# Optimization experiments

Hardware: AMD Instinct MI355X
Metric: run time of the kernel (lower is better)

The kernel has to match this reference:

```python
import jax, jax.numpy as jnp
import numpy as np

B, T, D = 8, 2048, 256  # batch, time segments, feature dim (a_dim=v_dim=hidden=out=256)
EPS = 1e-8


def _layer_norm(x, g, b, eps=1e-6):
    m = jnp.mean(x, axis=-1, keepdims=True)
    v = jnp.var(x, axis=-1, keepdims=True)
    return (x - m) * jax.lax.rsqrt(v + eps) * g + b


def setup_inputs() -> dict:
    key = jax.random.key(0)
    ks = jax.random.split(key, 9)
    xav = lambda k: jax.random.uniform(k, (D, D), jnp.float32, -1.0, 1.0) * np.sqrt(6.0 / (D + D))
    return {
        "a_fea": jax.random.normal(ks[0], (B, T, D), jnp.float32),
        "v_fea": jax.random.normal(ks[1], (B, T, D), jnp.float32),
        "thr_val": jnp.float32(0.099),
        "Wv1": xav(ks[2]), "Wv2": xav(ks[3]), "Wvfc": xav(ks[4]),
        "Wa1": xav(ks[5]), "Wa2": xav(ks[6]), "Wafc": xav(ks[7]),
        "ln_g": jnp.ones((D,), jnp.float32),
        "ln_b": jnp.zeros((D,), jnp.float32),
    }


def reference(a_fea, v_fea, thr_val, Wv1, Wv2, Wvfc, Wa1, Wa2, Wafc, ln_g, ln_b):
    relu = jax.nn.relu
    # branch projections (dropout is identity at eval); torch Linear: x @ W.T
    v1 = relu(jnp.einsum('btd,hd->bth', v_fea, Wv1))
    v2 = relu(jnp.einsum('btd,hd->bth', v_fea, Wv2))
    a1 = relu(jnp.einsum('btd,hd->bth', a_fea, Wa1))
    a2 = relu(jnp.einsum('btd,hd->bth', a_fea, Wa2))

    d = v2.shape[-1]
    # scaled cross-modal scores, ReLU'd  [B, Tv, Ta]
    beta_va = relu(jnp.einsum('btd,bsd->bts', v2, a1) / jnp.sqrt(jnp.float32(d)))
    # a->v scores taken BEFORE row-normalization of beta_va (as in torch code)
    beta_av = jnp.transpose(beta_va, (0, 2, 1))

    time = beta_va.shape[-1]
    thr = thr_val * 10.0 / time

    # normalize -> threshold sparsify -> renormalize (v attends to a)
    bn_va = beta_va / (jnp.sum(beta_va, axis=-1, keepdims=True) + EPS)
    g_va = jnp.where(bn_va > thr, bn_va, 0.0)
    g_va = g_va / (jnp.sum(g_va, axis=-1, keepdims=True) + EPS)

    # same for a attends to v
    bn_av = beta_av / (jnp.sum(beta_av, axis=-1, keepdims=True) + EPS)
    g_av = jnp.where(bn_av > thr, bn_av, 0.0)
    g_av = g_av / (jnp.sum(g_av, axis=-1, keepdims=True) + EPS)

    # vectorized form of the diagonal selection double-loop (batch element 0)
    pred = (jnp.diagonal(g_av[0]) > 0).astype(jnp.float32)  # [T]

    a_pos = jnp.einsum('bts,bsd->btd', g_va, a2)
    v_psp = v_fea + a_pos
    v_pos = jnp.einsum('bts,bsd->btd', g_av, v1)
    a_psp = a_fea + v_pos

    v_psp = _layer_norm(relu(jnp.einsum('btd,od->bto', v_psp, Wvfc)), ln_g, ln_b)
    a_psp = _layer_norm(relu(jnp.einsum('btd,od->bto', a_psp, Wafc)), ln_g, ln_b)
    a_v_fuse = 0.5 * (v_psp + a_psp)
    return a_v_fuse, v_psp, a_psp, pred
```

## Files before the change

### kernel.cpp

```cpp
#include <hip/hip_runtime.h>
#include <math.h>

#define TT 2048
#define DD 256
#define NBATCH 8
#define EPSF 1e-8f

typedef unsigned short u16;
typedef __attribute__((ext_vector_type(8))) short short8;
typedef __attribute__((ext_vector_type(4))) float f32x4;

__device__ __forceinline__ u16 f2bf(float x) {
    unsigned int u = __builtin_bit_cast(unsigned int, x);
    u += 0x7fffu + ((u >> 16) & 1u);
    return (u16)(u >> 16);
}
__device__ __forceinline__ float bf2f(u16 h) {
    return __builtin_bit_cast(float, (unsigned int)h << 16);
}

__device__ __forceinline__ int frag_dst(int row, int k) {
    return (((row >> 4) * 4 + (k >> 3)) * 16 + (row & 15)) * 8 + (k & 7);
}

template<int BR>
__device__ __forceinline__ void stage_tile(const u16* __restrict__ g, u16* s,
                                           int row0, int k0, int ldk, int tid)
{
    #pragma unroll
    for (int i = 0; i < BR / 64; ++i) {
        const int c = tid + 256 * i;
        const int row = c >> 2, q = c & 3;
        *(int4*)(s + frag_dst(row, q * 8)) =
            *(const int4*)(g + (long)(row0 + row) * ldk + k0 + q * 8);
    }
}

__global__ __launch_bounds__(256)
void proj_kernel(const u16* __restrict__ vfh, const u16* __restrict__ vfl,
                 const u16* __restrict__ afh, const u16* __restrict__ afl,
                 const u16* __restrict__ Wsp,
                 u16* __restrict__ v2h, u16* __restrict__ v2l,
                 u16* __restrict__ a1h, u16* __restrict__ a1l,
                 u16* __restrict__ v1T, u16* __restrict__ a2T)
{
    const int zz = blockIdx.z;
    const u16* Ah = (zz == 1 || zz == 3) ? afh : vfh;
    const u16* Al = (zz == 1 || zz == 3) ? afl : vfl;
    const int widx = (zz == 0) ? 2 : (zz == 1) ? 4 : (zz == 2) ? 0 : 6;
    const u16* Bh = Wsp + widx * DD * DD;
    const u16* Bl = Bh + DD * DD;
    const bool split = zz < 2;
    u16* Oh = (zz == 0) ? v2h : a1h;
    u16* Ol = (zz == 0) ? v2l : a1l;
    u16* OT = (zz == 2) ? v1T : a2T;

    __shared__ __align__(16) u16 Ah_s[64 * 32], Al_s[64 * 32];
    __shared__ __align__(16) u16 Bh_s[64 * 32], Bl_s[64 * 32];
    const int m0 = blockIdx.y * 64, n0 = blockIdx.x * 64;
    const int tid = threadIdx.x, lane = tid & 63, w = tid >> 6;
    const int wy = w >> 1, wx = w & 1;
    f32x4 acc[2][2] = {};

    for (int k0 = 0; k0 < DD; k0 += 32) {
        stage_tile<64>(Ah, Ah_s, m0, k0, DD, tid);
        stage_tile<64>(Al, Al_s, m0, k0, DD, tid);
        stage_tile<64>(Bh, Bh_s, n0, k0, DD, tid);
        stage_tile<64>(Bl, Bl_s, n0, k0, DD, tid);
        __syncthreads();
        short8 ah[2], al[2], bh[2], bl[2];
        #pragma unroll
        for (int i = 0; i < 2; ++i) {
            ah[i] = *(const short8*)(Ah_s + ((wy * 2 + i) * 64 + lane) * 8);
            al[i] = *(const short8*)(Al_s + ((wy * 2 + i) * 64 + lane) * 8);
        }
        #pragma unroll
        for (int j = 0; j < 2; ++j) {
            bh[j] = *(const short8*)(Bh_s + ((wx * 2 + j) * 64 + lane) * 8);
            bl[j] = *(const short8*)(Bl_s + ((wx * 2 + j) * 64 + lane) * 8);
        }
        #pragma unroll
        for (int i = 0; i < 2; ++i)
            #pragma unroll
            for (int j = 0; j < 2; ++j) {
                acc[i][j] = __builtin_amdgcn_mfma_f32_16x16x32_bf16(ah[i], bl[j], acc[i][j], 0, 0, 0);
                acc[i][j] = __builtin_amdgcn_mfma_f32_16x16x32_bf16(al[i], bh[j], acc[i][j], 0, 0, 0);
                acc[i][j] = __builtin_amdgcn_mfma_f32_16x16x32_bf16(ah[i], bh[j], acc[i][j], 0, 0, 0);
            }
        __syncthreads();
    }
    const int quad = lane >> 4, col = lane & 15;
    #pragma unroll
    for (int i = 0; i < 2; ++i)
        #pragma unroll
        for (int j = 0; j < 2; ++j) {
            const int c = n0 + (wx * 2 + j) * 16 + col;
            const int rbase = m0 + (wy * 2 + i) * 16 + quad * 4;
            if (split) {
                #pragma unroll
                for (int r = 0; r < 4; ++r) {
                    const float v = fmaxf(acc[i][j][r], 0.f);
                    const u16 h = f2bf(v);
                    Oh[(long)(rbase + r) * DD + c] = h;
                    Ol[(long)(rbase + r) * DD + c] = f2bf(v - bf2f(h));
                }
            } else {
                short4 pk;
                pk.x = (short)f2bf(fmaxf(acc[i][j][0], 0.f));
                pk.y = (short)f2bf(fmaxf(acc[i][j][1], 0.f));
                pk.z = (short)f2bf(fmaxf(acc[i][j][2], 0.f));
                pk.w = (short)f2bf(fmaxf(acc[i][j][3], 0.f));
                const int b = rbase >> 11, t = rbase & (TT - 1);
                *(short4*)(OT + ((long)b * DD + c) * TT + t) = pk;
            }
        }
}

__global__ __launch_bounds__(256)
void score_kernel(const u16* __restrict__ v2h, const u16* __restrict__ v2l,
                  const u16* __restrict__ a1h, const u16* __restrict__ a1l,
                  u16* __restrict__ beta, u16* __restrict__ betaT,
                  float* __restrict__ rs, float* __restrict__ cs)
{
    __shared__ __align__(16) u16 S[128 * 136];
    u16* Ah_s = S;
    u16* Al_s = S + 4096;
    u16* Bh_s = S + 8192;
    u16* Bl_s = S + 12288;
    const int z = blockIdx.z;
    const int m0 = blockIdx.y * 128, n0 = blockIdx.x * 128;
    const int tid = threadIdx.x, lane = tid & 63, w = tid >> 6;
    const int wy = w >> 1, wx = w & 1;
    const long zoff = (long)z * TT * DD;
    f32x4 acc[4][4] = {};

    for (int k0 = 0; k0 < DD; k0 += 32) {
        stage_tile<128>(v2h + zoff, Ah_s, m0, k0, DD, tid);
        stage_tile<128>(v2l + zoff, Al_s, m0, k0, DD, tid);
        stage_tile<128>(a1h + zoff, Bh_s, n0, k0, DD, tid);
        stage_tile<128>(a1l + zoff, Bl_s, n0, k0, DD, tid);
        __syncthreads();
        short8 ah[4], al[4], bh[4], bl[4];
        #pragma unroll
        for (int i = 0; i < 4; ++i) {
            ah[i] = *(const short8*)(Ah_s + ((wy * 4 + i) * 64 + lane) * 8);
            al[i] = *(const short8*)(Al_s + ((wy * 4 + i) * 64 + lane) * 8);
        }
        #pragma unroll
        for (int j = 0; j < 4; ++j) {
            bh[j] = *(const short8*)(Bh_s + ((wx * 4 + j) * 64 + lane) * 8);
            bl[j] = *(const short8*)(Bl_s + ((wx * 4 + j) * 64 + lane) * 8);
        }
        #pragma unroll
        for (int i = 0; i < 4; ++i)
            #pragma unroll
            for (int j = 0; j < 4; ++j) {
                acc[i][j] = __builtin_amdgcn_mfma_f32_16x16x32_bf16(ah[i], bl[j], acc[i][j], 0, 0, 0);
                acc[i][j] = __builtin_amdgcn_mfma_f32_16x16x32_bf16(al[i], bh[j], acc[i][j], 0, 0, 0);
                acc[i][j] = __builtin_amdgcn_mfma_f32_16x16x32_bf16(ah[i], bh[j], acc[i][j], 0, 0, 0);
            }
        __syncthreads();
    }

    const int quad = lane >> 4, col = lane & 15;
    const float scale = 1.f / 16.f;
    #pragma unroll
    for (int i = 0; i < 4; ++i)
        #pragma unroll
        for (int j = 0; j < 4; ++j) {
            const int c = n0 + (wx * 4 + j) * 16 + col;
            const int rbase = m0 + (wy * 4 + i) * 16 + quad * 4;
            #pragma unroll
            for (int r = 0; r < 4; ++r) {
                float v = fmaxf(acc[i][j][r] * scale, 0.f);
                acc[i][j][r] = v;
                beta[((long)z * TT + rbase + r) * TT + c] = f2bf(v);
            }
        }
    #pragma unroll
    for (int i = 0; i < 4; ++i)
        #pragma unroll
        for (int r = 0; r < 4; ++r) {
            float rp = 0.f;
            #pragma unroll
            for (int j = 0; j < 4; ++j) rp += acc[i][j][r];
            rp += __shfl_xor(rp, 1); rp += __shfl_xor(rp, 2);
            rp += __shfl_xor(rp, 4); rp += __shfl_xor(rp, 8);
            if (col == 0) {
                const int row = m0 + (wy * 4 + i) * 16 + quad * 4 + r;
                atomicAdd(&rs[(long)z * TT + row], rp);
            }
        }
    #pragma unroll
    for (int j = 0; j < 4; ++j) {
        float cp = 0.f;
        #pragma unroll
        for (int i = 0; i < 4; ++i)
            #pragma unroll
            for (int r = 0; r < 4; ++r) cp += acc[i][j][r];
        cp += __shfl_xor(cp, 16); cp += __shfl_xor(cp, 32);
        if (lane < 16) {
            const int c = n0 + (wx * 4 + j) * 16 + col;
            atomicAdd(&cs[(long)z * TT + c], cp);
        }
    }
    __syncthreads();
    #pragma unroll
    for (int i = 0; i < 4; ++i)
        #pragma unroll
        for (int j = 0; j < 4; ++j) {
            const int cl = (wx * 4 + j) * 16 + col;
            const int rl = (wy * 4 + i) * 16 + quad * 4;
            short4 pk;
            pk.x = (short)f2bf(acc[i][j][0]);
            pk.y = (short)f2bf(acc[i][j][1]);
            pk.z = (short)f2bf(acc[i][j][2]);
            pk.w = (short)f2bf(acc[i][j][3]);
            *(short4*)(S + cl * 136 + rl) = pk;
        }
    __syncthreads();
    #pragma unroll
    for (int it = 0; it < 8; ++it) {
        const int idx = tid + 256 * it;
        const int cl = idx >> 4, tq = idx & 15;
        const int4 v = *(const int4*)(S + cl * 136 + tq * 8);
        *(int4*)(betaT + ((long)z * TT + n0 + cl) * TT + m0 + tq * 8) = v;
    }
}

__global__ __launch_bounds__(512)
void pv_kernel(const u16* __restrict__ beta, const u16* __restrict__ betaT,
               const u16* __restrict__ a2T, const u16* __restrict__ v1T,
               const float* __restrict__ rs, const float* __restrict__ cs,
               const float* __restrict__ thrp,
               const float* __restrict__ v_fea, const float* __restrict__ a_fea,
               u16* __restrict__ yvin, u16* __restrict__ yain)
{
    __shared__ __align__(16) u16 A_s[128 * 32], B_s[256 * 32];
    __shared__ float sthr[128], sA[128], ssum[128];
    const int zz = blockIdx.x;
    const int m0 = blockIdx.y * 128;
    const int z = zz & 7;
    const bool av = zz >= 8;
    const u16* P      = av ? betaT : beta;
    const u16* VT     = av ? v1T : a2T;
    const float* sums = av ? cs : rs;
    const float* resid = av ? a_fea : v_fea;
    u16* outb         = av ? yain : yvin;

    const int tid = threadIdx.x, lane = tid & 63, w = tid >> 6;
    const int wy = w >> 2, wx = w & 3;
    const float thr = thrp[0] * 10.0f / (float)TT;
    if (tid < 128) {
        const float s = sums[(long)z * TT + m0 + tid];
        sA[tid] = s; sthr[tid] = thr * (s + EPSF); ssum[tid] = 0.f;
    }
    __syncthreads();
    f32x4 acc[4][4] = {};
    float rpart = 0.f;
    const int arow = tid >> 2, aq = tid & 3;
    const u16* Pp = P + ((long)z * TT + m0 + arow) * TT + aq * 8;
    const u16* V0 = VT + (long)z * DD * TT + (long)arow * TT + aq * 8;
    const u16* V1 = V0 + (long)128 * TT;

    int4 Ar  = *(const int4*)(Pp);
    int4 Br0 = *(const int4*)(V0);
    int4 Br1 = *(const int4*)(V1);

    for (int k0 = 0; k0 < TT; k0 += 32) {
        union { int4 v; u16 us[8]; } U;
        U.v = Ar;
        const float ct = sthr[arow];
        float ss = 0.f;
        #pragma unroll
        for (int t = 0; t < 8; ++t) {
            const float v = bf2f(U.us[t]);
            if (v > ct) ss += v; else U.us[t] = 0;
        }
        rpart += ss;
        *(int4*)(A_s + frag_dst(arow, aq * 8)) = U.v;
        *(int4*)(B_s + frag_dst(arow, aq * 8)) = Br0;
        *(int4*)(B_s + frag_dst(arow + 128, aq * 8)) = Br1;
        __syncthreads();
        const int kn = (k0 + 32 < TT) ? (k0 + 32) : k0;
        Ar  = *(const int4*)(Pp + kn);
        Br0 = *(const int4*)(V0 + kn);
        Br1 = *(const int4*)(V1 + kn);
        short8 a[4], b[4];
        #pragma unroll
        for (int i = 0; i < 4; ++i)
            a[i] = *(const short8*)(A_s + ((wy * 4 + i) * 64 + lane) * 8);
        #pragma unroll
        for (int j = 0; j < 4; ++j)
            b[j] = *(const short8*)(B_s + ((wx * 4 + j) * 64 + lane) * 8);
        #pragma unroll
        for (int i = 0; i < 4; ++i)
            #pragma unroll
            for (int j = 0; j < 4; ++j)
                acc[i][j] = __builtin_amdgcn_mfma_f32_16x16x32_bf16(a[i], b[j], acc[i][j], 0, 0, 0);
        __syncthreads();
    }
    atomicAdd(&ssum[arow], rpart);
    __syncthreads();

    const int quad = lane >> 4, col = lane & 15;
    #pragma unroll
    for (int i = 0; i < 4; ++i)
        #pragma unroll
        for (int j = 0; j < 4; ++j) {
            const int c = (wx * 4 + j) * 16 + col;
            #pragma unroll
            for (int r = 0; r < 4; ++r) {
                const int lrow = (wy * 4 + i) * 16 + quad * 4 + r;
                const int row = m0 + lrow;
                const float inv = 1.0f / (ssum[lrow] + EPSF * (sA[lrow] + EPSF));
                const float v = acc[i][j][r] * inv + resid[((long)z * TT + row) * DD + c];
                outb[((long)z * TT + row) * DD + c] = f2bf(v);
            }
        }
}

__global__ __launch_bounds__(256)
void fc_kernel(const u16* __restrict__ Ain, const u16* __restrict__ Wb,
               float* __restrict__ Cf)
{
    const int z = blockIdx.z;
    const u16* A = Ain + (size_t)z * (size_t)NBATCH * TT * DD;
    const u16* B = Wb + (size_t)z * DD * DD;
    float* C = Cf + (size_t)z * (size_t)NBATCH * TT * DD;
    __shared__ __align__(16) u16 A_s[128 * 32], B_s[64 * 32];
    const int m0 = blockIdx.y * 128, n0 = blockIdx.x * 64;
    const int tid = threadIdx.x, lane = tid & 63, w = tid >> 6;
    const int wy = w >> 1, wx = w & 1;
    f32x4 acc[4][2] = {};
    for (int k0 = 0; k0 < DD; k0 += 32) {
        stage_tile<128>(A, A_s, m0, k0, DD, tid);
        stage_tile<64>(B, B_s, n0, k0, DD, tid);
        __syncthreads();
        short8 a[4], b[2];
        #pragma unroll
        for (int i = 0; i < 4; ++i)
            a[i] = *(const short8*)(A_s + ((wy * 4 + i) * 64 + lane) * 8);
        #pragma unroll
        for (int j = 0; j < 2; ++j)
            b[j] = *(const short8*)(B_s + ((wx * 2 + j) * 64 + lane) * 8);
        #pragma unroll
        for (int i = 0; i < 4; ++i)
            #pragma unroll
            for (int j = 0; j < 2; ++j)
                acc[i][j] = __builtin_amdgcn_mfma_f32_16x16x32_bf16(a[i], b[j], acc[i][j], 0, 0, 0);
        __syncthreads();
    }
    const int quad = lane >> 4, col = lane & 15;
    #pragma unroll
    for (int i = 0; i < 4; ++i)
        #pragma unroll
        for (int j = 0; j < 2; ++j) {
            const int c = n0 + (wx * 2 + j) * 16 + col;
            #pragma unroll
            for (int r = 0; r < 4; ++r) {
                const int row = m0 + (wy * 4 + i) * 16 + quad * 4 + r;
                C[(long)row * DD + c] = fmaxf(acc[i][j][r], 0.f);
            }
        }
}

__global__ __launch_bounds__(256)
void pred_exact(const float* __restrict__ vf, const float* __restrict__ af,
                const float* __restrict__ Wv2, const float* __restrict__ Wa1,
                const float* __restrict__ cs, const float* __restrict__ thrp,
                float* __restrict__ pred)
{
    __shared__ float vs[8][260];
    __shared__ float as_[8][260];
    __shared__ float red[4][8];
    const int t0 = blockIdx.x * 8;
    const int tid = threadIdx.x;
    {
        const int i = tid >> 5, c = (tid & 31) * 8;
        *(float4*)&vs[i][c] = *(const float4*)(vf + (long)(t0 + i) * DD + c);
        *(float4*)&vs[i][c + 4] = *(const float4*)(vf + (long)(t0 + i) * DD + c + 4);
        *(float4*)&as_[i][c] = *(const float4*)(af + (long)(t0 + i) * DD + c);
        *(float4*)&as_[i][c + 4] = *(const float4*)(af + (long)(t0 + i) * DD + c + 4);
    }
    __syncthreads();
    const int j = tid;
    float av[8] = {0.f}, aa[8] = {0.f};
    for (int k = 0; k < DD; k += 4) {
        const float4 wv = *(const float4*)(Wv2 + (long)j * DD + k);
        const float4 wa = *(const float4*)(Wa1 + (long)j * DD + k);
        #pragma unroll
        for (int i = 0; i < 8; ++i) {
            const float4 x = *(const float4*)&vs[i][k];
            av[i] += wv.x * x.x + wv.y * x.y + wv.z * x.z + wv.w * x.w;
            const float4 y = *(const float4*)&as_[i][k];
            aa[i] += wa.x * y.x + wa.y * y.y + wa.z * y.z + wa.w * y.w;
        }
    }
    float p[8];
    #pragma unroll
    for (int i = 0; i < 8; ++i)
        p[i] = fmaxf(av[i], 0.f) * fmaxf(aa[i], 0.f);
    #pragma unroll
    for (int off = 32; off > 0; off >>= 1)
        #pragma unroll
        for (int i = 0; i < 8; ++i) p[i] += __shfl_xor(p[i], off);
    const int lane = tid & 63, wv_ = tid >> 6;
    if (lane == 0)
        #pragma unroll
        for (int i = 0; i < 8; ++i) red[wv_][i] = p[i];
    __syncthreads();
    if (tid < 8) {
        float d = red[0][tid] + red[1][tid] + red[2][tid] + red[3][tid];
        d = fmaxf(d * (1.f / 16.f), 0.f);
        const float thr = thrp[0] * 10.0f / (float)TT;
        pred[t0 + tid] = (d > thr * (cs[t0 + tid] + EPSF)) ? 1.0f : 0.0f;
    }
}

__global__ __launch_bounds__(256)
void split_feat(const float* __restrict__ vf, const float* __restrict__ af,
                u16* __restrict__ vfh, u16* __restrict__ vfl,
                u16* __restrict__ afh, u16* __restrict__ afl)
{
    const long i4 = ((long)blockIdx.x * 256 + threadIdx.x) * 4;
    const float* src = blockIdx.y ? af : vf;
    u16* dh = blockIdx.y ? afh : vfh;
    u16* dl = blockIdx.y ? afl : vfl;
    float4 a = *(const float4*)(src + i4);
    ushort4 h4, l4; u16 h;
    h = f2bf(a.x); h4.x = h; l4.x = f2bf(a.x - bf2f(h));
    h = f2bf(a.y); h4.y = h; l4.y = f2bf(a.y - bf2f(h));
    h = f2bf(a.z); h4.z = h; l4.z = f2bf(a.z - bf2f(h));
    h = f2bf(a.w); h4.w = h; l4.w = f2bf(a.w - bf2f(h));
    *(ushort4*)(dh + i4) = h4;
    *(ushort4*)(dl + i4) = l4;
}

__global__ __launch_bounds__(256)
void split_w(const float* __restrict__ w0, const float* __restrict__ w1,
             const float* __restrict__ w2, const float* __restrict__ w3,
             const float* __restrict__ w4, const float* __restrict__ w5,
             u16* __restrict__ out)
{
    const int t = blockIdx.y;
    const float* w = (t == 0) ? w0 : (t == 1) ? w1 : (t == 2) ? w2
                   : (t == 3) ? w3 : (t == 4) ? w4 : w5;
    const int i4 = (blockIdx.x * 256 + threadIdx.x) * 4;
    float4 a = *(const float4*)(w + i4);
    if (t < 4) {
        u16* oh = out + (size_t)t * 2 * DD * DD;
        u16* ol = oh + DD * DD;
        ushort4 h4, l4; u16 h;
        h = f2bf(a.x); h4.x = h; l4.x = f2bf(a.x - bf2f(h));
        h = f2bf(a.y); h4.y = h; l4.y = f2bf(a.y - bf2f(h));
        h = f2bf(a.z); h4.z = h; l4.z = f2bf(a.z - bf2f(h));
        h = f2bf(a.w); h4.w = h; l4.w = f2bf(a.w - bf2f(h));
        *(ushort4*)(oh + i4) = h4;
        *(ushort4*)(ol + i4) = l4;
    } else {
        u16* ob = out + (size_t)8 * DD * DD + (size_t)(t - 4) * DD * DD;
        ushort4 o;
        o.x = f2bf(a.x); o.y = f2bf(a.y); o.z = f2bf(a.z); o.w = f2bf(a.w);
        *(ushort4*)(ob + i4) = o;
    }
}

__global__ __launch_bounds__(256)
void ln_fuse_kernel(const float* __restrict__ yv, const float* __restrict__ ya,
                    const float* __restrict__ g, const float* __restrict__ b,
                    float* __restrict__ fuse, float* __restrict__ vpsp,
                    float* __restrict__ apsp)
{
    const long row = (long)blockIdx.x * 4 + (threadIdx.x >> 6);
    const int lane = threadIdx.x & 63;
    const float4 xv = *(const float4*)(yv + row * DD + lane * 4);
    const float4 xa = *(const float4*)(ya + row * DD + lane * 4);
    float sv = xv.x + xv.y + xv.z + xv.w;
    float sa = xa.x + xa.y + xa.z + xa.w;
    #pragma unroll
    for (int off = 32; off > 0; off >>= 1) {
        sv += __shfl_xor(sv, off);
        sa += __shfl_xor(sa, off);
    }
    const float mv = sv * (1.f / 256.f);
    const float ma = sa * (1.f / 256.f);
    const float dv0 = xv.x - mv, dv1 = xv.y - mv, dv2 = xv.z - mv, dv3 = xv.w - mv;
    const float da0 = xa.x - ma, da1 = xa.y - ma, da2 = xa.z - ma, da3 = xa.w - ma;
    float qv = dv0 * dv0 + dv1 * dv1 + dv2 * dv2 + dv3 * dv3;
    float qa = da0 * da0 + da1 * da1 + da2 * da2 + da3 * da3;
    #pragma unroll
    for (int off = 32; off > 0; off >>= 1) {
        qv += __shfl_xor(qv, off);
        qa += __shfl_xor(qa, off);
    }
    const float rv = rsqrtf(qv * (1.f / 256.f) + 1e-6f);
    const float ra = rsqrtf(qa * (1.f / 256.f) + 1e-6f);
    const float4 gg = *(const float4*)(g + lane * 4);
    const float4 bb = *(const float4*)(b + lane * 4);
    float4 ov, oa, of;
    ov.x = dv0 * rv * gg.x + bb.x; ov.y = dv1 * rv * gg.y + bb.y;
    ov.z = dv2 * rv * gg.z + bb.z; ov.w = dv3 * rv * gg.w + bb.w;
    oa.x = da0 * ra * gg.x + bb.x; oa.y = da1 * ra * gg.y + bb.y;
    oa.z = da2 * ra * gg.z + bb.z; oa.w = da3 * ra * gg.w + bb.w;
    of.x = 0.5f * (ov.x + oa.x); of.y = 0.5f * (ov.y + oa.y);
    of.z = 0.5f * (ov.z + oa.z); of.w = 0.5f * (ov.w + oa.w);
    *(float4*)(vpsp + row * DD + lane * 4) = ov;
    *(float4*)(apsp + row * DD + lane * 4) = oa;
    *(float4*)(fuse + row * DD + lane * 4) = of;
}

extern "C" void kernel_launch(void* const* d_in, const int* in_sizes, int n_in,
                              void* d_out, int out_size, void* d_ws, size_t ws_size,
                              hipStream_t stream)
{
    const float* a_fea = (const float*)d_in[0];
    const float* v_fea = (const float*)d_in[1];
    const float* thrp  = (const float*)d_in[2];
    const float* Wv1   = (const float*)d_in[3];
    const float* Wv2   = (const float*)d_in[4];
    const float* Wvfc  = (const float*)d_in[5];
    const float* Wa1   = (const float*)d_in[6];
    const float* Wa2   = (const float*)d_in[7];
    const float* Wafc  = (const float*)d_in[8];
    const float* lng   = (const float*)d_in[9];
    const float* lnb   = (const float*)d_in[10];

    const long MT = (long)NBATCH * TT;
    float* out_fuse = (float*)d_out;
    float* out_vpsp = out_fuse + MT * DD;
    float* out_apsp = out_vpsp + MT * DD;
    float* out_pred = out_apsp + MT * DD;

    char* ws = (char*)d_ws;
    const size_t fb = (size_t)MT * DD * sizeof(u16);
    const size_t sumB = (size_t)MT * sizeof(float);
    u16* v2h  = (u16*)(ws + 0 * fb);
    u16* v2l  = (u16*)(ws + 1 * fb);
    u16* a1h  = (u16*)(ws + 2 * fb);
    u16* a1l  = (u16*)(ws + 3 * fb);
    u16* yvin = (u16*)(ws + 4 * fb);
    u16* yain = (u16*)(ws + 5 * fb);
    u16* v1T  = (u16*)(ws + 6 * fb);
    u16* a2T  = (u16*)(ws + 7 * fb);
    char* p = ws + 8 * fb;
    float* rs = (float*)(p + 0 * sumB);
    float* cs = (float*)(p + 1 * sumB);
    u16* Wsp  = (u16*)(p + 2 * sumB);
    char* q = p + 2 * sumB + 10 * DD * DD * sizeof(u16);
    const size_t betaB = (size_t)NBATCH * TT * TT * sizeof(u16);
    u16* beta  = (u16*)q;
    u16* betaT = (u16*)(q + betaB);
    u16* vfh = (u16*)q;
    u16* vfl = vfh + MT * DD;
    u16* afh = vfl + MT * DD;
    u16* afl = afh + MT * DD;
    float* yv = (float*)(ws + 0 * fb);
    float* ya = (float*)(ws + 2 * fb);

    hipMemsetAsync(rs, 0, 2 * sumB, stream);

    const dim3 blk(256, 1, 1);

    split_feat<<<dim3((unsigned)(MT * DD / 1024), 2, 1), blk, 0, stream>>>(
        v_fea, a_fea, vfh, vfl, afh, afl);
    split_w<<<dim3(DD * DD / 1024, 6, 1), blk, 0, stream>>>(
        Wv1, Wv2, Wa1, Wa2, Wvfc, Wafc, Wsp);

    proj_kernel<<<dim3(DD / 64, (unsigned)(MT / 64), 4), blk, 0, stream>>>(
        vfh, vfl, afh, afl, Wsp, v2h, v2l, a1h, a1l, v1T, a2T);

    score_kernel<<<dim3(TT / 128, TT / 128, NBATCH), blk, 0, stream>>>(
        v2h, v2l, a1h, a1l, beta, betaT, rs, cs);
    pred_exact<<<dim3(TT / 8, 1, 1), blk, 0, stream>>>(
        v_fea, a_fea, Wv2, Wa1, cs, thrp, out_pred);

    pv_kernel<<<dim3(2 * NBATCH, TT / 128, 1), dim3(512, 1, 1), 0, stream>>>(
        beta, betaT, a2T, v1T, rs, cs, thrp, v_fea, a_fea, yvin, yain);

    fc_kernel<<<dim3(DD / 64, (unsigned)(MT / 128), 2), blk, 0, stream>>>(
        yvin, Wsp + 8 * DD * DD, yv);
    ln_fuse_kernel<<<dim3((unsigned)(MT / 4), 1, 1), blk, 0, stream>>>(
        yv, ya, lng, lnb, out_fuse, out_vpsp, out_apsp);
}
```

Baseline: 443.4 us.

## Swizzle LDS fragment layout, prefetch score tiles in registers, stage beta stores

Adds an XOR swizzle to the LDS fragment layout, used consistently by every GEMM stage and read, to cut LDS bank conflicts on the int4 stores. The score kernel now preloads the next k-slice of its global tiles into registers while the MFMAs run on the current one, so loads overlap compute. It also writes the bf16 beta tile through LDS and then stores it with coalesced 16-byte rows, replacing scattered 2-byte stores. This costs more registers in the score kernel and one extra barrier.

```diff
diff --git a/kernel.cpp b/kernel.cpp
--- a/kernel.cpp
+++ b/kernel.cpp
@@ -23,6 +23,8 @@
     return (((row >> 4) * 4 + (k >> 3)) * 16 + (row & 15)) * 8 + (k & 7);
 }
 
+__device__ __forceinline__ int swz(int i) { return i ^ ((i >> 2) & 32); }
+
 template<int BR>
 __device__ __forceinline__ void stage_tile(const u16* __restrict__ g, u16* s,
                                            int row0, int k0, int ldk, int tid)
@@ -31,7 +33,7 @@
     for (int i = 0; i < BR / 64; ++i) {
         const int c = tid + 256 * i;
         const int row = c >> 2, q = c & 3;
-        *(int4*)(s + frag_dst(row, q * 8)) =
+        *(int4*)(s + swz(frag_dst(row, q * 8))) =
             *(const int4*)(g + (long)(row0 + row) * ldk + k0 + q * 8);
     }
 }
@@ -71,13 +73,13 @@
         short8 ah[2], al[2], bh[2], bl[2];
         #pragma unroll
         for (int i = 0; i < 2; ++i) {
-            ah[i] = *(const short8*)(Ah_s + ((wy * 2 + i) * 64 + lane) * 8);
-            al[i] = *(const short8*)(Al_s + ((wy * 2 + i) * 64 + lane) * 8);
+            ah[i] = *(const short8*)(Ah_s + swz(((wy * 2 + i) * 64 + lane) * 8));
+            al[i] = *(const short8*)(Al_s + swz(((wy * 2 + i) * 64 + lane) * 8));
         }
         #pragma unroll
         for (int j = 0; j < 2; ++j) {
-            bh[j] = *(const short8*)(Bh_s + ((wx * 2 + j) * 64 + lane) * 8);
-            bl[j] = *(const short8*)(Bl_s + ((wx * 2 + j) * 64 + lane) * 8);
+            bh[j] = *(const short8*)(Bh_s + swz(((wx * 2 + j) * 64 + lane) * 8));
+            bl[j] = *(const short8*)(Bl_s + swz(((wx * 2 + j) * 64 + lane) * 8));
         }
         #pragma unroll
         for (int i = 0; i < 2; ++i)
@@ -134,22 +136,41 @@
     const long zoff = (long)z * TT * DD;
     f32x4 acc[4][4] = {};
 
+    const int prow = tid >> 2, pq = tid & 3;
+    const int d0 = swz(frag_dst(prow, pq * 8));
+    const int d1 = swz(frag_dst(prow + 64, pq * 8));
+    const u16* gAh = v2h + zoff + (long)(m0 + prow) * DD + pq * 8;
+    const u16* gAl = v2l + zoff + (long)(m0 + prow) * DD + pq * 8;
+    const u16* gBh = a1h + zoff + (long)(n0 + prow) * DD + pq * 8;
+    const u16* gBl = a1l + zoff + (long)(n0 + prow) * DD + pq * 8;
+    const int rstep = 64 * DD;
+
+    int4 rAh0 = *(const int4*)(gAh), rAh1 = *(const int4*)(gAh + rstep);
+    int4 rAl0 = *(const int4*)(gAl), rAl1 = *(const int4*)(gAl + rstep);
+    int4 rBh0 = *(const int4*)(gBh), rBh1 = *(const int4*)(gBh + rstep);
+    int4 rBl0 = *(const int4*)(gBl), rBl1 = *(const int4*)(gBl + rstep);
+
     for (int k0 = 0; k0 < DD; k0 += 32) {
-        stage_tile<128>(v2h + zoff, Ah_s, m0, k0, DD, tid);
-        stage_tile<128>(v2l + zoff, Al_s, m0, k0, DD, tid);
-        stage_tile<128>(a1h + zoff, Bh_s, n0, k0, DD, tid);
-        stage_tile<128>(a1l + zoff, Bl_s, n0, k0, DD, tid);
-        __syncthreads();
+        *(int4*)(Ah_s + d0) = rAh0; *(int4*)(Ah_s + d1) = rAh1;
+        *(int4*)(Al_s + d0) = rAl0; *(int4*)(Al_s + d1) = rAl1;
+        *(int4*)(Bh_s + d0) = rBh0; *(int4*)(Bh_s + d1) = rBh1;
+        *(int4*)(Bl_s + d0) = rBl0; *(int4*)(Bl_s + d1) = rBl1;
+        __syncthreads();
+        const int kn = (k0 + 32 < DD) ? k0 + 32 : 0;
+        rAh0 = *(const int4*)(gAh + kn); rAh1 = *(const int4*)(gAh + rstep + kn);
+        rAl0 = *(const int4*)(gAl + kn); rAl1 = *(const int4*)(gAl + rstep + kn);
+        rBh0 = *(const int4*)(gBh + kn); rBh1 = *(const int4*)(gBh + rstep + kn);
+        rBl0 = *(const int4*)(gBl + kn); rBl1 = *(const int4*)(gBl + rstep + kn);
         short8 ah[4], al[4], bh[4], bl[4];
         #pragma unroll
         for (int i = 0; i < 4; ++i) {
-            ah[i] = *(const short8*)(Ah_s + ((wy * 4 + i) * 64 + lane) * 8);
-            al[i] = *(const short8*)(Al_s + ((wy * 4 + i) * 64 + lane) * 8);
+            ah[i] = *(const short8*)(Ah_s + swz(((wy * 4 + i) * 64 + lane) * 8));
+            al[i] = *(const short8*)(Al_s + swz(((wy * 4 + i) * 64 + lane) * 8));
         }
         #pragma unroll
         for (int j = 0; j < 4; ++j) {
-            bh[j] = *(const short8*)(Bh_s + ((wx * 4 + j) * 64 + lane) * 8);
-            bl[j] = *(const short8*)(Bl_s + ((wx * 4 + j) * 64 + lane) * 8);
+            bh[j] = *(const short8*)(Bh_s + swz(((wx * 4 + j) * 64 + lane) * 8));
+            bl[j] = *(const short8*)(Bl_s + swz(((wx * 4 + j) * 64 + lane) * 8));
         }
         #pragma unroll
         for (int i = 0; i < 4; ++i)
@@ -167,16 +188,30 @@
     #pragma unroll
     for (int i = 0; i < 4; ++i)
         #pragma unroll
+        for (int j = 0; j < 4; ++j)
+            #pragma unroll
+            for (int r = 0; r < 4; ++r)
+                acc[i][j][r] = fmaxf(acc[i][j][r] * scale, 0.f);
+
+    #pragma unroll
+    for (int i = 0; i < 4; ++i) {
+        const int rl = (wy * 4 + i) * 16 + quad * 4;
+        #pragma unroll
         for (int j = 0; j < 4; ++j) {
-            const int c = n0 + (wx * 4 + j) * 16 + col;
-            const int rbase = m0 + (wy * 4 + i) * 16 + quad * 4;
-            #pragma unroll
-            for (int r = 0; r < 4; ++r) {
-                float v = fmaxf(acc[i][j][r] * scale, 0.f);
-                acc[i][j][r] = v;
-                beta[((long)z * TT + rbase + r) * TT + c] = f2bf(v);
-            }
-        }
+            const int cl = (wx * 4 + j) * 16 + col;
+            #pragma unroll
+            for (int r = 0; r < 4; ++r)
+                S[(rl + r) * 136 + cl] = f2bf(acc[i][j][r]);
+        }
+    }
+    __syncthreads();
+    #pragma unroll
+    for (int it = 0; it < 8; ++it) {
+        const int idx = tid + 256 * it;
+        const int rl = idx >> 4, cq = idx & 15;
+        const int4 v = *(const int4*)(S + rl * 136 + cq * 8);
+        *(int4*)(beta + ((long)z * TT + m0 + rl) * TT + n0 + cq * 8) = v;
+    }
     #pragma unroll
     for (int i = 0; i < 4; ++i)
         #pragma unroll
@@ -262,6 +297,8 @@
     const u16* Pp = P + ((long)z * TT + m0 + arow) * TT + aq * 8;
     const u16* V0 = VT + (long)z * DD * TT + (long)arow * TT + aq * 8;
     const u16* V1 = V0 + (long)128 * TT;
+    const int da  = swz(frag_dst(arow, aq * 8));
+    const int db1 = swz(frag_dst(arow + 128, aq * 8));
 
     int4 Ar  = *(const int4*)(Pp);
     int4 Br0 = *(const int4*)(V0);
@@ -278,9 +315,9 @@
             if (v > ct) ss += v; else U.us[t] = 0;
         }
         rpart += ss;
-        *(int4*)(A_s + frag_dst(arow, aq * 8)) = U.v;
-        *(int4*)(B_s + frag_dst(arow, aq * 8)) = Br0;
-        *(int4*)(B_s + frag_dst(arow + 128, aq * 8)) = Br1;
+        *(int4*)(A_s + da) = U.v;
+        *(int4*)(B_s + da) = Br0;
+        *(int4*)(B_s + db1) = Br1;
         __syncthreads();
         const int kn = (k0 + 32 < TT) ? (k0 + 32) : k0;
         Ar  = *(const int4*)(Pp + kn);
@@ -289,10 +326,10 @@
         short8 a[4], b[4];
         #pragma unroll
         for (int i = 0; i < 4; ++i)
-            a[i] = *(const short8*)(A_s + ((wy * 4 + i) * 64 + lane) * 8);
+            a[i] = *(const short8*)(A_s + swz(((wy * 4 + i) * 64 + lane) * 8));
         #pragma unroll
         for (int j = 0; j < 4; ++j)
-            b[j] = *(const short8*)(B_s + ((wx * 4 + j) * 64 + lane) * 8);
+            b[j] = *(const short8*)(B_s + swz(((wx * 4 + j) * 64 + lane) * 8));
         #pragma unroll
         for (int i = 0; i < 4; ++i)
             #pragma unroll
@@ -340,10 +377,10 @@
         short8 a[4], b[2];
         #pragma unroll
         for (int i = 0; i < 4; ++i)
-            a[i] = *(const short8*)(A_s + ((wy * 4 + i) * 64 + lane) * 8);
+            a[i] = *(const short8*)(A_s + swz(((wy * 4 + i) * 64 + lane) * 8));
         #pragma unroll
         for (int j = 0; j < 2; ++j)
-            b[j] = *(const short8*)(B_s + ((wx * 2 + j) * 64 + lane) * 8);
+            b[j] = *(const short8*)(B_s + swz(((wx * 2 + j) * 64 + lane) * 8));
         #pragma unroll
         for (int i = 0; i < 4; ++i)
             #pragma unroll
```

Result: faster. 430.2 us (-3.0%).
